# Kernel tuning notes

Measured on AMD Instinct MI355X. Metric: run time of the kernel, lower is better.

Reference implementation:

```python
import jax, jax.numpy as jnp
import numpy as np

PAD_VAL = -999
N_TYPES = 8
D_IN, D_FF, D_FFC = 512, 1024, 512
B, S = 64, 512


def setup_inputs() -> dict:
    key = jax.random.key(0)
    ks = jax.random.split(key, 6)
    sc = 0.02
    return {
        "x": jax.random.normal(ks[0], (B, S, D_IN), dtype=jnp.float32),
        "sc_types": jax.random.randint(ks[1], (B, S), 0, N_TYPES, dtype=jnp.int64),
        "W_pre": jax.random.normal(ks[2], (D_IN, D_FF), dtype=jnp.float32) * sc,
        "W_types": jax.random.normal(ks[3], (N_TYPES, D_FF, D_IN), dtype=jnp.float32) * sc,
        "W_c1": jax.random.normal(ks[4], (D_IN, D_FFC), dtype=jnp.float32) * sc,
        "W_c2": jax.random.normal(ks[5], (D_FFC, 1), dtype=jnp.float32) * sc,
    }


def reference(x, sc_types, W_pre, W_types, W_c1, W_c2):
    # flatten tokens: [B*S, d_in], [B*S]
    x = x.reshape(-1, x.shape[-1])
    t = sc_types.reshape(-1)
    # (inputs contain no PAD_VAL tokens, so the pad mask is all-True and the
    # gather x[mask] is the identity; shapes stay static)
    x_ = jax.nn.relu(x @ W_pre)                       # [N, d_ff]
    # hard type routing: select per-type MLP output for each token
    x_types = jnp.zeros_like(x)
    for i in range(N_TYPES):
        yi = jax.nn.relu(x_ @ W_types[i])             # [N, d_in]
        x_types = jnp.where((t == i)[:, None], yi, x_types)
    x = x + x_types                                    # residual combine
    h = jax.nn.relu(x @ W_c1)                          # [N, d_ffc]
    return h @ W_c2                                    # [N, 1]
```

## Files before the change

### kernel.cpp

```cpp
#include <hip/hip_runtime.h>
#include <stdint.h>

#define N_TOK 32768
#define DIN   512
#define DFF   1024
#define MPAD  33792

__device__ __forceinline__ int rotk(int k, int row) {
    return (k & ~127) + (((k & 127) + ((row & 15) << 3)) & 127);
}

typedef __attribute__((ext_vector_type(8))) short bf16x8;
typedef __attribute__((ext_vector_type(4))) float f32x4;

__device__ __forceinline__ unsigned short f2bf(float f) {
    union { float f; unsigned int u; } v; v.f = f;
    unsigned int u = v.u;
    return (unsigned short)((u + 0x7FFFu + ((u >> 16) & 1u)) >> 16);
}
__device__ __forceinline__ float bf2f(unsigned int bits) {
    union { unsigned int u; float f; } v; v.u = bits << 16; return v.f;
}
__device__ __forceinline__ unsigned int pk4_fp8(float a, float b, float c, float d) {
    int v = __builtin_amdgcn_cvt_pk_fp8_f32(a, b, 0, false);
    v = __builtin_amdgcn_cvt_pk_fp8_f32(c, d, v, true);
    return (unsigned int)v;
}
__device__ __forceinline__ unsigned char f2fp8(float a) {
    return (unsigned char)(__builtin_amdgcn_cvt_pk_fp8_f32(a, a, 0, false) & 0xFF);
}

__device__ __forceinline__ void async16(const void* g, void* l) {
    __builtin_amdgcn_global_load_lds(
        (const __attribute__((address_space(1))) void*)g,
        (__attribute__((address_space(3))) void*)l, 16, 0, 0);
}

__global__ void prep_kernel(const float* __restrict__ x,
                            unsigned short* __restrict__ Xb,
                            unsigned char* __restrict__ Xb8,
                            const int* __restrict__ types,
                            int* __restrict__ blockhist,
                            const float* __restrict__ Wp,
                            const float* __restrict__ Wt,
                            const float* __restrict__ Wc,
                            unsigned char* __restrict__ Wp8,
                            unsigned char* __restrict__ Wt8,
                            unsigned short* __restrict__ WcT,
                            int* __restrict__ perm) {
    __shared__ float tile[32][33];
    __shared__ int lc[8];
    const int b = blockIdx.x, tid = threadIdx.x;
    if (b < 16384) {
        const int i = b * 1024 + tid * 4;
        float4 v = *(const float4*)(x + i);
        ushort4 o;
        o.x = f2bf(v.x); o.y = f2bf(v.y); o.z = f2bf(v.z); o.w = f2bf(v.w);
        *(ushort4*)(Xb + i) = o;
        const int row = i >> 9;
        const int k   = i & 511;
        *(unsigned int*)(Xb8 + (size_t)row * DIN + rotk(k, row)) = pk4_fp8(v.x, v.y, v.z, v.w);
        if (b < 64) {
            if (tid < 8) lc[tid] = 0;
            __syncthreads();
            atomicAdd(&lc[types[b * 512 + tid]], 1);
            atomicAdd(&lc[types[b * 512 + 256 + tid]], 1);
            __syncthreads();
            if (tid < 8) blockhist[b * 8 + tid] = lc[tid];
        }
    } else if (b < 26624) {
        const int r = b - 16384;
        const int z = r >> 10;
        const int bx = r & 31, by = (r >> 5) & 31;
        const int tx = tid & 31, ty = tid >> 5;
        const float* s; int K, N;
        if (z == 0)      { s = Wp;                          K = 512;  N = 1024; }
        else if (z <= 8) { s = Wt + (size_t)(z-1)*DIN*DFF;  K = 1024; N = 512; }
        else             { s = Wc;                          K = 512;  N = 512; }
        const int n0 = bx * 32, k0 = by * 32;
        if (n0 >= N || k0 >= K) return;
        for (int i = ty; i < 32; i += 8)
            tile[i][tx] = s[(size_t)(k0 + i) * N + n0 + tx];
        __syncthreads();
        if (z <= 8) {
            unsigned char* d = (z == 0) ? Wp8 : (Wt8 + (size_t)(z-1)*DIN*DFF);
            const int nl = tid >> 3;
            const int k4 = (tid & 7) << 2;
            const int n  = n0 + nl;
            const int kk = k0 + k4;
            unsigned int pk = pk4_fp8(tile[k4 + 0][nl] * 64.f, tile[k4 + 1][nl] * 64.f,
                                      tile[k4 + 2][nl] * 64.f, tile[k4 + 3][nl] * 64.f);
            *(unsigned int*)(d + (size_t)n * K + rotk(kk, n)) = pk;
        } else {
            for (int i = ty; i < 32; i += 8)
                WcT[(size_t)(n0 + i) * K + k0 + tx] = f2bf(tile[tx][i]);
        }
    } else {
        perm[(b - 26624) * 256 + tid] = -1;
    }
}

__global__ void scatter_kernel(const int* __restrict__ types,
                               const int* __restrict__ blockhist,
                               int* __restrict__ perm,
                               int* __restrict__ invperm,
                               float* __restrict__ outz,
                               int* __restrict__ po_out) {
    __shared__ int tots[8], base[8], fill[8];
    const int blk = blockIdx.x;
    const int tid = threadIdx.x;
    const int i = blk * 512 + tid;
    outz[i] = 0.f;
    int pre = 0;
    if (tid < 8) {
        int total = 0;
        for (int j = 0; j < 64; j++) {
            int v = blockhist[j * 8 + tid];
            if (j < blk) pre += v;
            total += v;
        }
        tots[tid] = total;
    }
    __syncthreads();
    if (tid < 8) {
        int off = 0, pob = 0;
        #pragma unroll
        for (int t2 = 0; t2 < 8; t2++) {
            if (t2 == tid) pob = off;
            off += ((tots[t2] + 127) >> 7) << 7;
        }
        base[tid] = pob + pre;
        fill[tid] = 0;
        if (blk == 0) {
            po_out[tid] = pob;
            if (tid == 0) po_out[8] = off;
        }
    }
    __syncthreads();
    const int t = types[i];
    const int r = atomicAdd(&fill[t], 1);
    const int p = base[t] + r;
    perm[p] = i;
    invperm[i] = p;
}

template <int MODE>
__global__ __launch_bounds__(1024, 8)
void gemm_fp8_kernel(const unsigned char* __restrict__ A,
                     const unsigned char* __restrict__ B,
                     void* __restrict__ Cout,
                     const unsigned short* __restrict__ xres,
                     const int* __restrict__ pmap,
                     const int* __restrict__ po,
                     int K, int ldA) {
    __shared__ unsigned char As[128 * 128];
    __shared__ unsigned char Bs[128 * 128];
    __shared__ int ptile[128];

    const int tid  = threadIdx.x;
    const int wave = tid >> 6;
    const int lane = tid & 63;
    const int quad = lane >> 4;
    const int tl   = lane & 15;
    int m0, n0;
    if constexpr (MODE == 1) {
        const int sid = (blockIdx.x & 7) * 132 + (blockIdx.x >> 3);
        m0 = (sid >> 2) * 128;
        n0 = (sid & 3) * 128;
    } else {
        const int sid = (blockIdx.x & 7) * 256 + (blockIdx.x >> 3);
        m0 = (sid >> 3) * 128;
        n0 = (sid & 7) * 128;
    }
    const int wm = (wave >> 2) * 32;
    const int wn = (wave & 3) * 32;

    const unsigned char* Bp = B;
    if constexpr (MODE == 1) {
        if (m0 >= po[8]) return;
        int bsel = 0;
        #pragma unroll
        for (int i = 1; i < 8; i++) bsel += (m0 >= po[i]) ? 1 : 0;
        Bp = B + (size_t)bsel * (DIN * DFF);
    }
    if (tid < 128) ptile[tid] = pmap[m0 + tid];

    f32x4 acc[2][2];
    #pragma unroll
    for (int i = 0; i < 2; i++)
        #pragma unroll
        for (int j = 0; j < 2; j++)
            acc[i][j] = (f32x4){0.f, 0.f, 0.f, 0.f};

    const int arow = tid >> 3;
    const int aj   = (tid & 7) * 16;
    const unsigned char* aptr = A + (size_t)(m0 + arow) * ldA + aj;
    const unsigned char* bptr = Bp + (size_t)(n0 + arow) * K + aj;

    for (int k0 = 0; k0 < K; k0 += 128) {
        __syncthreads();
        async16(aptr + k0, (char*)As + tid * 16);
        async16(bptr + k0, (char*)Bs + tid * 16);
        __syncthreads();

        #pragma unroll
        for (int ks = 0; ks < 4; ks++) {
            long af[2], bfr[2];
            const int o = (ks * 32 + quad * 8 + tl * 8) & 127;
            #pragma unroll
            for (int t = 0; t < 2; t++)
                af[t] = *(const long*)(As + (wm + t * 16 + tl) * 128 + o);
            #pragma unroll
            for (int t = 0; t < 2; t++)
                bfr[t] = *(const long*)(Bs + (wn + t * 16 + tl) * 128 + o);
            #pragma unroll
            for (int mt = 0; mt < 2; mt++)
                #pragma unroll
                for (int nt = 0; nt < 2; nt++)
                    acc[mt][nt] = __builtin_amdgcn_mfma_f32_16x16x32_fp8_fp8(
                        bfr[nt], af[mt], acc[mt][nt], 0, 0, 0);
        }
    }

    if constexpr (MODE == 0) {
        unsigned char* C8 = (unsigned char*)Cout;
        #pragma unroll
        for (int mt = 0; mt < 2; mt++) {
            const int p = ptile[wm + mt * 16 + tl];
            const size_t rowbase = (size_t)p * DFF;
            const int prot = (p & 15) << 3;
            #pragma unroll
            for (int nt = 0; nt < 2; nt++) {
                const int off = wn + nt * 16 + quad * 4;
                unsigned int pk = pk4_fp8(fmaxf(acc[mt][nt][0], 0.f) * 0.125f,
                                          fmaxf(acc[mt][nt][1], 0.f) * 0.125f,
                                          fmaxf(acc[mt][nt][2], 0.f) * 0.125f,
                                          fmaxf(acc[mt][nt][3], 0.f) * 0.125f);
                const int phys = (off & ~127) + (((off & 127) + prot) & 127);
                *(unsigned int*)(C8 + rowbase + n0 + phys) = pk;
            }
        }
    } else {
        unsigned short* Cb = (unsigned short*)Cout;
        int toks[2];
        #pragma unroll
        for (int mt = 0; mt < 2; mt++) toks[mt] = ptile[wm + mt * 16 + tl];
        ushort4 rv[2][2];
        #pragma unroll
        for (int mt = 0; mt < 2; mt++) {
            if (toks[mt] < 0) continue;
            const size_t rowbase = (size_t)toks[mt] * DIN;
            #pragma unroll
            for (int nt = 0; nt < 2; nt++)
                rv[mt][nt] = *(const ushort4*)(xres + rowbase + n0 + wn + nt * 16 + quad * 4);
        }
        #pragma unroll
        for (int mt = 0; mt < 2; mt++) {
            if (toks[mt] < 0) continue;
            const size_t rowbase = (size_t)toks[mt] * DIN;
            #pragma unroll
            for (int nt = 0; nt < 2; nt++) {
                const int ncol = n0 + wn + nt * 16 + quad * 4;
                ushort4 o;
                o.x = f2bf(bf2f(rv[mt][nt].x) + fmaxf(acc[mt][nt][0], 0.f) * 0.001953125f);
                o.y = f2bf(bf2f(rv[mt][nt].y) + fmaxf(acc[mt][nt][1], 0.f) * 0.001953125f);
                o.z = f2bf(bf2f(rv[mt][nt].z) + fmaxf(acc[mt][nt][2], 0.f) * 0.001953125f);
                o.w = f2bf(bf2f(rv[mt][nt].w) + fmaxf(acc[mt][nt][3], 0.f) * 0.001953125f);
                *(ushort4*)(Cb + rowbase + ncol) = o;
            }
        }
    }
}

__global__ __launch_bounds__(512, 4)
void gemm3_kernel(const unsigned short* __restrict__ A,
                  const unsigned short* __restrict__ B,
                  const float* __restrict__ w2,
                  float* __restrict__ outp,
                  int K, int ldA) {
    __shared__ unsigned short As[128 * 64];
    __shared__ unsigned short Bs[256 * 64];

    const int tid  = threadIdx.x;
    const int wave = tid >> 6;
    const int lane = tid & 63;
    const int quad = lane >> 4;
    const int tl   = lane & 15;
    const int sid = (blockIdx.x & 7) * 64 + (blockIdx.x >> 3);
    const int m0 = (sid >> 1) * 128;
    const int n0 = (sid & 1) * 256;
    const int wm = (wave & 1) * 64;
    const int wn = (wave >> 1) * 64;

    f32x4 acc[4][4];
    #pragma unroll
    for (int i = 0; i < 4; i++)
        #pragma unroll
        for (int j = 0; j < 4; j++)
            acc[i][j] = (f32x4){0.f, 0.f, 0.f, 0.f};

    for (int k0 = 0; k0 < K; k0 += 64) {
        __syncthreads();
        #pragma unroll
        for (int i = 0; i < 2; i++) {
            const int c   = (i * 8 + wave) * 64 + lane;
            const int row = c >> 3;
            const int gj  = (c & 7) ^ (row & 7);
            async16(A + (size_t)(m0 + row) * ldA + k0 + gj * 8, (char*)As + (size_t)c * 16);
        }
        #pragma unroll
        for (int i = 0; i < 4; i++) {
            const int c   = (i * 8 + wave) * 64 + lane;
            const int row = c >> 3;
            const int gj  = (c & 7) ^ (row & 7);
            async16(B + (size_t)(n0 + row) * K + k0 + gj * 8, (char*)Bs + (size_t)c * 16);
        }
        __syncthreads();

        #pragma unroll
        for (int ks = 0; ks < 2; ks++) {
            bf16x8 af[4], bfr[4];
            const int jc = ks * 4 + quad;
            #pragma unroll
            for (int t = 0; t < 4; t++) {
                const int r = wm + t * 16 + tl;
                af[t] = *(const bf16x8*)(As + (r * 8 + (jc ^ (r & 7))) * 8);
            }
            #pragma unroll
            for (int t = 0; t < 4; t++) {
                const int r = wn + t * 16 + tl;
                bfr[t] = *(const bf16x8*)(Bs + (r * 8 + (jc ^ (r & 7))) * 8);
            }
            #pragma unroll
            for (int mt = 0; mt < 4; mt++)
                #pragma unroll
                for (int nt = 0; nt < 4; nt++)
                    acc[mt][nt] = __builtin_amdgcn_mfma_f32_16x16x32_bf16(
                        bfr[nt], af[mt], acc[mt][nt], 0, 0, 0);
        }
    }

    float4 w2v[4];
    #pragma unroll
    for (int nt = 0; nt < 4; nt++)
        w2v[nt] = *(const float4*)(w2 + n0 + wn + nt * 16 + quad * 4);
    #pragma unroll
    for (int mt = 0; mt < 4; mt++) {
        float s = 0.f;
        #pragma unroll
        for (int nt = 0; nt < 4; nt++) {
            s += fmaxf(acc[mt][nt][0], 0.f) * w2v[nt].x;
            s += fmaxf(acc[mt][nt][1], 0.f) * w2v[nt].y;
            s += fmaxf(acc[mt][nt][2], 0.f) * w2v[nt].z;
            s += fmaxf(acc[mt][nt][3], 0.f) * w2v[nt].w;
        }
        s += __shfl_down(s, 32);
        s += __shfl_down(s, 16);
        if (lane < 16) atomicAdd(&outp[m0 + wm + mt * 16 + lane], s);
    }
}

extern "C" void kernel_launch(void* const* d_in, const int* in_sizes, int n_in,
                              void* d_out, int out_size, void* d_ws, size_t ws_size,
                              hipStream_t stream) {
    const float* x      = (const float*)d_in[0];
    const int*   types  = (const int*)d_in[1];
    const float* W_pre  = (const float*)d_in[2];
    const float* W_types= (const float*)d_in[3];
    const float* W_c1   = (const float*)d_in[4];
    const float* W_c2   = (const float*)d_in[5];
    float* out = (float*)d_out;

    char* ws = (char*)d_ws;
    unsigned short* Xb  = (unsigned short*)(ws);
    unsigned char*  Xff8= (unsigned char*)(ws + 33554432ull);
    unsigned char*  Xb8 = (unsigned char*)(ws + 68157440ull);
    unsigned char*  Wp8 = (unsigned char*)(ws + 84934656ull);
    unsigned char*  Wt8 = (unsigned char*)(ws + 85458944ull);
    unsigned short* WcT = (unsigned short*)(ws + 89653248ull);
    int* perm           = (int*)(ws + 90177536ull);
    int* invperm        = (int*)(ws + 90312704ull);
    int* po             = (int*)(ws + 90443776ull);
    int* blockhist      = po + 16;

    prep_kernel<<<26756, 256, 0, stream>>>(x, Xb, Xb8, types, blockhist,
                                           W_pre, W_types, W_c1, Wp8, Wt8, WcT, perm);
    scatter_kernel<<<64, 512, 0, stream>>>(types, blockhist, perm, invperm, out, po);
    gemm_fp8_kernel<0><<<2048, 1024, 0, stream>>>(
        Xb8, Wp8, Xff8, nullptr, invperm, nullptr, 512, 512);
    gemm_fp8_kernel<1><<<1056, 1024, 0, stream>>>(
        Xff8, Wt8, Xb, Xb, perm, po, 1024, 1024);
    gemm3_kernel<<<512, 512, 0, stream>>>(
        Xb, WcT, W_c2, out, 512, 512);
}
```

Baseline: 233.7 us.

## Use gfx950 16x16x128 scaled FP8 MFMA with 256-thread blocks and 64x64 wave tiles

Replaces the 16x16x32 FP8 MFMA with the MI355X 16x16x128 f8f6f4 scaled MFMA, using neutral scales of 127. Blocks shrink from 1024 to 256 threads, so each wave computes a 64x64 sub-tile with a 4x4 accumulator grid and gets more fragment reuse per LDS read. The first GEMM's grid becomes a plain 2D layout instead of the swizzled block order. The cost is higher register pressure and fewer waves per block to hide latency, and the L2-friendly block ordering is dropped for MODE 0.

```diff
diff --git a/kernel.cpp b/kernel.cpp
--- a/kernel.cpp
+++ b/kernel.cpp
@@ -12,6 +12,9 @@
 
 typedef __attribute__((ext_vector_type(8))) short bf16x8;
 typedef __attribute__((ext_vector_type(4))) float f32x4;
+typedef __attribute__((ext_vector_type(8))) int   i32x8;
+
+union frag8 { long l[4]; i32x8 v; };
 
 __device__ __forceinline__ unsigned short f2bf(float f) {
     union { float f; unsigned int u; } v; v.f = f;
@@ -145,7 +148,7 @@
 }
 
 template <int MODE>
-__global__ __launch_bounds__(1024, 8)
+__global__ __launch_bounds__(256, 3)
 void gemm_fp8_kernel(const unsigned char* __restrict__ A,
                      const unsigned char* __restrict__ B,
                      void* __restrict__ Cout,
@@ -168,12 +171,11 @@
         m0 = (sid >> 2) * 128;
         n0 = (sid & 3) * 128;
     } else {
-        const int sid = (blockIdx.x & 7) * 256 + (blockIdx.x >> 3);
-        m0 = (sid >> 3) * 128;
-        n0 = (sid & 7) * 128;
-    }
-    const int wm = (wave >> 2) * 32;
-    const int wn = (wave & 3) * 32;
+        m0 = blockIdx.y * 128;
+        n0 = blockIdx.x * 128;
+    }
+    const int wm = (wave & 1) * 64;
+    const int wn = (wave >> 1) * 64;
 
     const unsigned char* Bp = B;
     if constexpr (MODE == 1) {
@@ -185,52 +187,65 @@
     }
     if (tid < 128) ptile[tid] = pmap[m0 + tid];
 
-    f32x4 acc[2][2];
+    f32x4 acc[4][4];
     #pragma unroll
-    for (int i = 0; i < 2; i++)
-        #pragma unroll
-        for (int j = 0; j < 2; j++)
+    for (int i = 0; i < 4; i++)
+        #pragma unroll
+        for (int j = 0; j < 4; j++)
             acc[i][j] = (f32x4){0.f, 0.f, 0.f, 0.f};
-
-    const int arow = tid >> 3;
-    const int aj   = (tid & 7) * 16;
-    const unsigned char* aptr = A + (size_t)(m0 + arow) * ldA + aj;
-    const unsigned char* bptr = Bp + (size_t)(n0 + arow) * K + aj;
 
     for (int k0 = 0; k0 < K; k0 += 128) {
         __syncthreads();
-        async16(aptr + k0, (char*)As + tid * 16);
-        async16(bptr + k0, (char*)Bs + tid * 16);
+        #pragma unroll
+        for (int i = 0; i < 4; i++) {
+            const int c   = (i * 4 + wave) * 64 + lane;
+            const int row = c >> 3;
+            const int j   = c & 7;
+            async16(A + (size_t)(m0 + row) * ldA + k0 + j * 16, (char*)As + (size_t)c * 16);
+        }
+        #pragma unroll
+        for (int i = 0; i < 4; i++) {
+            const int c   = (i * 4 + wave) * 64 + lane;
+            const int row = c >> 3;
+            const int j   = c & 7;
+            async16(Bp + (size_t)(n0 + row) * K + k0 + j * 16, (char*)Bs + (size_t)c * 16);
+        }
         __syncthreads();
 
-        #pragma unroll
-        for (int ks = 0; ks < 4; ks++) {
-            long af[2], bfr[2];
-            const int o = (ks * 32 + quad * 8 + tl * 8) & 127;
-            #pragma unroll
-            for (int t = 0; t < 2; t++)
-                af[t] = *(const long*)(As + (wm + t * 16 + tl) * 128 + o);
-            #pragma unroll
-            for (int t = 0; t < 2; t++)
-                bfr[t] = *(const long*)(Bs + (wn + t * 16 + tl) * 128 + o);
-            #pragma unroll
-            for (int mt = 0; mt < 2; mt++)
-                #pragma unroll
-                for (int nt = 0; nt < 2; nt++)
-                    acc[mt][nt] = __builtin_amdgcn_mfma_f32_16x16x32_fp8_fp8(
-                        bfr[nt], af[mt], acc[mt][nt], 0, 0, 0);
+        frag8 bfr[4];
+        #pragma unroll
+        for (int nt = 0; nt < 4; nt++) {
+            const unsigned char* bp = Bs + (wn + nt * 16 + tl) * 128;
+            #pragma unroll
+            for (int j = 0; j < 4; j++)
+                bfr[nt].l[j] = *(const long*)(bp + ((quad * 32 + j * 8 + tl * 8) & 127));
+        }
+        #pragma unroll
+        for (int mt = 0; mt < 4; mt++) {
+            frag8 af;
+            const unsigned char* ap = As + (wm + mt * 16 + tl) * 128;
+            #pragma unroll
+            for (int j = 0; j < 4; j++)
+                af.l[j] = *(const long*)(ap + ((quad * 32 + j * 8 + tl * 8) & 127));
+            #pragma unroll
+            for (int nt = 0; nt < 4; nt++)
+                acc[mt][nt] = __builtin_amdgcn_mfma_scale_f32_16x16x128_f8f6f4(
+                    bfr[nt].v, af.v, acc[mt][nt],
+                    0, 0,
+                    0, 127,
+                    0, 127);
         }
     }
 
     if constexpr (MODE == 0) {
         unsigned char* C8 = (unsigned char*)Cout;
         #pragma unroll
-        for (int mt = 0; mt < 2; mt++) {
+        for (int mt = 0; mt < 4; mt++) {
             const int p = ptile[wm + mt * 16 + tl];
             const size_t rowbase = (size_t)p * DFF;
             const int prot = (p & 15) << 3;
             #pragma unroll
-            for (int nt = 0; nt < 2; nt++) {
+            for (int nt = 0; nt < 4; nt++) {
                 const int off = wn + nt * 16 + quad * 4;
                 unsigned int pk = pk4_fp8(fmaxf(acc[mt][nt][0], 0.f) * 0.125f,
                                           fmaxf(acc[mt][nt][1], 0.f) * 0.125f,
@@ -242,24 +257,24 @@
         }
     } else {
         unsigned short* Cb = (unsigned short*)Cout;
-        int toks[2];
-        #pragma unroll
-        for (int mt = 0; mt < 2; mt++) toks[mt] = ptile[wm + mt * 16 + tl];
-        ushort4 rv[2][2];
-        #pragma unroll
-        for (int mt = 0; mt < 2; mt++) {
+        int toks[4];
+        #pragma unroll
+        for (int mt = 0; mt < 4; mt++) toks[mt] = ptile[wm + mt * 16 + tl];
+        ushort4 rv[4][4];
+        #pragma unroll
+        for (int mt = 0; mt < 4; mt++) {
             if (toks[mt] < 0) continue;
             const size_t rowbase = (size_t)toks[mt] * DIN;
             #pragma unroll
-            for (int nt = 0; nt < 2; nt++)
+            for (int nt = 0; nt < 4; nt++)
                 rv[mt][nt] = *(const ushort4*)(xres + rowbase + n0 + wn + nt * 16 + quad * 4);
         }
         #pragma unroll
-        for (int mt = 0; mt < 2; mt++) {
+        for (int mt = 0; mt < 4; mt++) {
             if (toks[mt] < 0) continue;
             const size_t rowbase = (size_t)toks[mt] * DIN;
             #pragma unroll
-            for (int nt = 0; nt < 2; nt++) {
+            for (int nt = 0; nt < 4; nt++) {
                 const int ncol = n0 + wn + nt * 16 + quad * 4;
                 ushort4 o;
                 o.x = f2bf(bf2f(rv[mt][nt].x) + fmaxf(acc[mt][nt][0], 0.f) * 0.001953125f);
@@ -386,9 +401,9 @@
     prep_kernel<<<26756, 256, 0, stream>>>(x, Xb, Xb8, types, blockhist,
                                            W_pre, W_types, W_c1, Wp8, Wt8, WcT, perm);
     scatter_kernel<<<64, 512, 0, stream>>>(types, blockhist, perm, invperm, out, po);
-    gemm_fp8_kernel<0><<<2048, 1024, 0, stream>>>(
+    gemm_fp8_kernel<0><<<dim3(DFF / 128, N_TOK / 128), 256, 0, stream>>>(
         Xb8, Wp8, Xff8, nullptr, invperm, nullptr, 512, 512);
-    gemm_fp8_kernel<1><<<1056, 1024, 0, stream>>>(
+    gemm_fp8_kernel<1><<<1056, 256, 0, stream>>>(
         Xff8, Wt8, Xb, Xb, perm, po, 1024, 1024);
     gemm3_kernel<<<512, 512, 0, stream>>>(
         Xb, WcT, W_c2, out, 512, 512);
```

Measured after the change: 224.9 us. 3.8% less time.
